# Performance work log

Hardware: AMD Instinct MI355X
Metric: run time of the kernel (lower is better)

## Reference

```python
import jax, jax.numpy as jnp
import numpy as np

N, E, R, B, H, C = 50000, 1600000, 50, 30, 16, 4


def setup_inputs() -> dict:
    key = jax.random.key(0)
    ks = jax.random.split(key, 12)
    edge_index = jax.random.randint(ks[0], (2, E), 0, N, dtype=jnp.int64)
    edge_type = jax.random.randint(ks[1], (E,), 0, R, dtype=jnp.int64)
    edge_norm = jax.random.uniform(ks[2], (E,), dtype=jnp.float32)
    s = 0.1
    basis1 = jax.random.normal(ks[3], (B, N, H), dtype=jnp.float32) * s
    comp1 = jax.random.normal(ks[4], (R, B), dtype=jnp.float32) * s
    root1 = jax.random.normal(ks[5], (N, H), dtype=jnp.float32) * s
    bias1 = jnp.zeros((H,), dtype=jnp.float32)
    basis2 = jax.random.normal(ks[6], (B, H, C), dtype=jnp.float32) * s
    comp2 = jax.random.normal(ks[7], (R, B), dtype=jnp.float32) * s
    root2 = jax.random.normal(ks[8], (H, C), dtype=jnp.float32) * s
    bias2 = jnp.zeros((C,), dtype=jnp.float32)
    return {
        "edge_index": edge_index, "edge_type": edge_type, "edge_norm": edge_norm,
        "basis1": basis1, "comp1": comp1, "root1": root1, "bias1": bias1,
        "basis2": basis2, "comp2": comp2, "root2": root2, "bias2": bias2,
    }


def _scatter_mean(msg, dst, n):
    # mean aggregation over destination nodes (PyG RGCNConv aggr='mean')
    summed = jnp.zeros((n, msg.shape[1]), dtype=msg.dtype).at[dst].add(msg)
    cnt = jnp.zeros((n,), dtype=msg.dtype).at[dst].add(1.0)
    return summed / jnp.maximum(cnt, 1.0)[:, None]


def reference(edge_index, edge_type, edge_norm, basis1, comp1, root1, bias1,
              basis2, comp2, root2, bias2):
    # edge_norm is accepted but unused, matching the original forward
    src, dst = edge_index[0], edge_index[1]
    n = root1.shape[0]
    # ---- layer 1: x is None -> per-(relation, src-node) weight row lookup ----
    w1 = jnp.einsum('rb,bnh->rnh', comp1, basis1)       # [R, N, H]
    msg1 = w1[edge_type, src]                           # [E, H] gather
    x = _scatter_mean(msg1, dst, n) + root1 + bias1      # root added directly (x=None)
    x = jax.nn.relu(x)
    # ---- layer 2: standard basis-decomposed RGCN on dense features ----
    w2 = jnp.einsum('rb,bhc->rhc', comp2, basis2)       # [R, H, C]
    msg2 = jnp.einsum('eh,ehc->ec', x[src], w2[edge_type])  # per-edge transform
    out = _scatter_mean(msg2, dst, n) + x @ root2 + bias2
    return jax.nn.log_softmax(out, axis=1)
```

## Files before the change

### kernel.cpp

```cpp
#include <hip/hip_runtime.h>
#include <math.h>

#define N_NODES 50000
#define E_EDGES 1600000
#define R_REL   50
#define B_BAS   30
#define H_DIM   16
#define C_DIM   4
#define NH      (N_NODES * H_DIM)

#define NSLICE      8
#define SLICE_NODES (N_NODES / NSLICE)

#define FRONT_BLOCKS (NH / 256)
#define EDGES_PER_FRONT (E_EDGES / FRONT_BLOCKS)

__global__ __launch_bounds__(256) void k_front(const float* __restrict__ basis1,
                                               const float* __restrict__ comp1,
                                               float* __restrict__ w1,
                                               const int* __restrict__ ei,
                                               int* __restrict__ cnt_i) {
    {
        const int ebase = blockIdx.x * EDGES_PER_FRONT + threadIdx.x;
        atomicAdd(&cnt_i[ei[E_EDGES + ebase]], 1);
        atomicAdd(&cnt_i[ei[E_EDGES + ebase + 256]], 1);
    }

    const int idx = blockIdx.x * 256 + threadIdx.x;
    float bv[B_BAS];
#pragma unroll
    for (int b = 0; b < B_BAS; ++b) bv[b] = basis1[b * NH + idx];

    for (int r = 0; r < R_REL; ++r) {
        float acc = 0.f;
#pragma unroll
        for (int b = 0; b < B_BAS; ++b) acc += comp1[r * B_BAS + b] * bv[b];
        w1[(size_t)r * NH + idx] = acc;
    }
}

__global__ __launch_bounds__(256) void k_scan_part(const int* __restrict__ cnt_i,
                                                   int* __restrict__ part,
                                                   int* __restrict__ bsum) {
    const int i = blockIdx.x * 256 + threadIdx.x;
    const int lane = threadIdx.x & 63;
    const int wid = threadIdx.x >> 6;
    const int v = (i < N_NODES) ? cnt_i[i] : 0;
    int s = v;
#pragma unroll
    for (int d = 1; d < 64; d <<= 1) {
        int t = __shfl_up(s, d, 64);
        if (lane >= d) s += t;
    }
    __shared__ int wsum[4];
    if (lane == 63) wsum[wid] = s;
    __syncthreads();
    int woff = 0;
    for (int w = 0; w < wid; ++w) woff += wsum[w];
    if (i < N_NODES) part[i] = s - v + woff;
    if (threadIdx.x == 255) bsum[blockIdx.x] = woff + s;
}

__global__ __launch_bounds__(256) void k_scan_tops(const int* __restrict__ bsum,
                                                   int* __restrict__ boff,
                                                   const float* __restrict__ basis2,
                                                   const float* __restrict__ comp2,
                                                   float* __restrict__ w2) {
    const int NB = (N_NODES + 255) / 256;
    const int lane = threadIdx.x & 63;
    const int wid = threadIdx.x >> 6;
    const int v = (threadIdx.x < NB) ? bsum[threadIdx.x] : 0;
    int s = v;
#pragma unroll
    for (int d = 1; d < 64; d <<= 1) {
        int t = __shfl_up(s, d, 64);
        if (lane >= d) s += t;
    }
    __shared__ int wsum[4];
    if (lane == 63) wsum[wid] = s;
    __syncthreads();
    int woff = 0;
    for (int w = 0; w < wid; ++w) woff += wsum[w];
    if (threadIdx.x < NB) boff[threadIdx.x] = s - v + woff;

    const int HC = H_DIM * C_DIM;
    for (int idx = threadIdx.x; idx < R_REL * HC; idx += 256) {
        const int r = idx / HC;
        const int hc = idx % HC;
        float acc = 0.f;
#pragma unroll
        for (int b = 0; b < B_BAS; ++b)
            acc += comp2[r * B_BAS + b] * basis2[b * HC + hc];
        w2[idx] = acc;
    }
}

__global__ __launch_bounds__(256) void k_scan_add(const int* __restrict__ part,
                                                  const int* __restrict__ boff,
                                                  int* __restrict__ off,
                                                  int* __restrict__ cursor) {
    const int i = blockIdx.x * 256 + threadIdx.x;
    if (i < N_NODES) {
        const int o = part[i] + boff[blockIdx.x];
        off[i] = o;
        cursor[i] = o;
    }
    if (i == 0) off[N_NODES] = E_EDGES;
}

__global__ __launch_bounds__(256) void k_bucket(const int* __restrict__ ei,
                                                const int* __restrict__ et,
                                                int* __restrict__ cursor,
                                                unsigned* __restrict__ rec) {
    const int chunk = blockIdx.x >> 3;
    const int slice = blockIdx.x & (NSLICE - 1);
    const int lo = slice * SLICE_NODES;

    const int e = chunk * 256 + threadIdx.x;
    if (e >= E_EDGES) return;
    const int dst = __builtin_nontemporal_load(&ei[E_EDGES + e]);
    if ((unsigned)(dst - lo) >= (unsigned)SLICE_NODES) return;

    const int src = __builtin_nontemporal_load(&ei[e]);
    const int r = __builtin_nontemporal_load(&et[e]);
    const int pos = atomicAdd(&cursor[dst], 1);
    rec[pos] = (unsigned)src | ((unsigned)r << 16);
}

__global__ __launch_bounds__(256) void k_agg1x(const unsigned* __restrict__ rec,
                                               const int* __restrict__ off,
                                               const float* __restrict__ w1,
                                               const float* __restrict__ root1,
                                               const float* __restrict__ bias1,
                                               float* __restrict__ x) {
    const int wid = threadIdx.x >> 6;
    const int lane = threadIdx.x & 63;
    const int dst = blockIdx.x * 4 + wid;
    const int h = lane & 15;
    const int sub = lane >> 4;
    const int e0 = off[dst], e1 = off[dst + 1];

    float acc = 0.f;
    for (int e = e0 + sub; e < e1; e += 16) {
        unsigned p[4];
#pragma unroll
        for (int j = 0; j < 4; ++j) {
            const int ej = e + j * 4;
            p[j] = (ej < e1) ? rec[ej] : 0xFFFFFFFFu;
        }
#pragma unroll
        for (int j = 0; j < 4; ++j) {
            if (p[j] != 0xFFFFFFFFu) {
                const int src = (int)(p[j] & 0xFFFFu);
                const int r = (int)(p[j] >> 16);
                acc += w1[(size_t)r * NH + src * H_DIM + h];
            }
        }
    }
    acc += __shfl_xor(acc, 16, 64);
    acc += __shfl_xor(acc, 32, 64);

    if (sub == 0) {
        const float c = fmaxf((float)(e1 - e0), 1.f);
        const float v = acc / c + root1[dst * H_DIM + h] + bias1[h];
        x[dst * H_DIM + h] = fmaxf(v, 0.f);
    }
}

__global__ __launch_bounds__(256) void k_agg2out(const unsigned* __restrict__ rec,
                                                 const int* __restrict__ off,
                                                 const float* __restrict__ x,
                                                 const float* __restrict__ w2,
                                                 const float* __restrict__ root2,
                                                 const float* __restrict__ bias2,
                                                 float* __restrict__ out) {
    const int wid = threadIdx.x >> 6;
    const int lane = threadIdx.x & 63;
    const int dst = blockIdx.x * 4 + wid;
    const int h = lane & 15;
    const int sub = lane >> 4;
    const int e0 = off[dst], e1 = off[dst + 1];

    float a0 = 0.f, a1 = 0.f, a2 = 0.f, a3 = 0.f;
    for (int e = e0 + sub; e < e1; e += 16) {
        unsigned p[4];
#pragma unroll
        for (int j = 0; j < 4; ++j) {
            const int ej = e + j * 4;
            p[j] = (ej < e1) ? rec[ej] : 0xFFFFFFFFu;
        }
#pragma unroll
        for (int j = 0; j < 4; ++j) {
            if (p[j] != 0xFFFFFFFFu) {
                const int src = (int)(p[j] & 0xFFFFu);
                const int r = (int)(p[j] >> 16);
                const float xv = x[src * H_DIM + h];
                const float4 w = *(const float4*)(w2 + r * (H_DIM * C_DIM) + h * C_DIM);
                a0 += xv * w.x; a1 += xv * w.y; a2 += xv * w.z; a3 += xv * w.w;
            }
        }
    }
#pragma unroll
    for (int d = 1; d < 64; d <<= 1) {
        a0 += __shfl_xor(a0, d, 64);
        a1 += __shfl_xor(a1, d, 64);
        a2 += __shfl_xor(a2, d, 64);
        a3 += __shfl_xor(a3, d, 64);
    }

    if (lane == 0) {
        const float c = fmaxf((float)(e1 - e0), 1.f);
        float y0 = a0 / c + bias2[0];
        float y1 = a1 / c + bias2[1];
        float y2 = a2 / c + bias2[2];
        float y3 = a3 / c + bias2[3];
#pragma unroll
        for (int hh = 0; hh < H_DIM; ++hh) {
            const float xv = x[dst * H_DIM + hh];
            const float4 w = *(const float4*)(root2 + hh * C_DIM);
            y0 += xv * w.x; y1 += xv * w.y; y2 += xv * w.z; y3 += xv * w.w;
        }
        const float m = fmaxf(fmaxf(y0, y1), fmaxf(y2, y3));
        const float s = expf(y0 - m) + expf(y1 - m) + expf(y2 - m) + expf(y3 - m);
        const float lse = m + logf(s);
        out[dst * 4 + 0] = y0 - lse;
        out[dst * 4 + 1] = y1 - lse;
        out[dst * 4 + 2] = y2 - lse;
        out[dst * 4 + 3] = y3 - lse;
    }
}

extern "C" void kernel_launch(void* const* d_in, const int* in_sizes, int n_in,
                              void* d_out, int out_size, void* d_ws, size_t ws_size,
                              hipStream_t stream) {
    const int*   edge_index = (const int*)d_in[0];
    const int*   edge_type  = (const int*)d_in[1];
    const float* basis1 = (const float*)d_in[3];
    const float* comp1  = (const float*)d_in[4];
    const float* root1  = (const float*)d_in[5];
    const float* bias1  = (const float*)d_in[6];
    const float* basis2 = (const float*)d_in[7];
    const float* comp2  = (const float*)d_in[8];
    const float* root2  = (const float*)d_in[9];
    const float* bias2  = (const float*)d_in[10];

    float* out = (float*)d_out;

    char* ws = (char*)d_ws;
    size_t o = 0;
    auto take = [&](size_t bytes) { char* p = ws + o; o += (bytes + 15) & ~(size_t)15; return p; };

    float*    w1     = (float*)   take((size_t)R_REL * NH * sizeof(float));
    unsigned* rec    = (unsigned*)take((size_t)E_EDGES * sizeof(unsigned));
    float*    x      = (float*)   take((size_t)NH * sizeof(float));
    int*      part   = (int*)x;
    int*      off    = (int*)     take((size_t)(N_NODES + 1) * sizeof(int));
    int*      cnt_i  = (int*)     take((size_t)N_NODES * sizeof(int));
    int*      cursor = (int*)     take((size_t)N_NODES * sizeof(int));
    float*    w2     = (float*)   take((size_t)R_REL * H_DIM * C_DIM * sizeof(float));
    int*      bsum   = (int*)     take(256 * sizeof(int));
    int*      boff   = (int*)     take(256 * sizeof(int));
    (void)ws_size;

    const int NB = (N_NODES + 255) / 256;

    hipMemsetAsync(cnt_i, 0, (size_t)N_NODES * sizeof(int), stream);

    k_front<<<FRONT_BLOCKS, 256, 0, stream>>>(basis1, comp1, w1, edge_index, cnt_i);

    k_scan_part<<<NB, 256, 0, stream>>>(cnt_i, part, bsum);
    k_scan_tops<<<1, 256, 0, stream>>>(bsum, boff, basis2, comp2, w2);
    k_scan_add<<<NB, 256, 0, stream>>>(part, boff, off, cursor);
    {
        const int chunks = (E_EDGES + 255) / 256;
        k_bucket<<<chunks * NSLICE, 256, 0, stream>>>(edge_index, edge_type, cursor, rec);
    }

    k_agg1x<<<N_NODES / 4, 256, 0, stream>>>(rec, off, w1, root1, bias1, x);

    k_agg2out<<<N_NODES / 4, 256, 0, stream>>>(rec, off, x, w2, root2, bias2, out);
}
```

Baseline: 412.1 us.

## Vectorize w1 basis contraction with float4 and split relations across block groups

The front kernel now processes four elements per thread with float4 loads and stores, and splits the 50 relations into 5 groups of 10 handled by separate blocks. Each thread keeps 10 float4 accumulators and streams over the basis instead of holding all 30 basis values. The degree-count atomics are redistributed to match the new block count. The goal is wider memory transactions and more parallelism for the bandwidth-bound w1 write, at the cost of reading basis1 five times.

```diff
diff --git a/kernel.cpp b/kernel.cpp
--- a/kernel.cpp
+++ b/kernel.cpp
@@ -8,35 +8,60 @@
 #define H_DIM   16
 #define C_DIM   4
 #define NH      (N_NODES * H_DIM)
+#define NH4     (NH / 4)
 
 #define NSLICE      8
 #define SLICE_NODES (N_NODES / NSLICE)
 
-#define FRONT_BLOCKS (NH / 256)
-#define EDGES_PER_FRONT (E_EDGES / FRONT_BLOCKS)
-
-__global__ __launch_bounds__(256) void k_front(const float* __restrict__ basis1,
-                                               const float* __restrict__ comp1,
-                                               float* __restrict__ w1,
-                                               const int* __restrict__ ei,
-                                               int* __restrict__ cnt_i) {
+#define R_GROUPS     5
+#define R_PER_GROUP  10
+#define IDX_BLOCKS   ((NH4 + 255) / 256)
+#define FRONT_BLOCKS (IDX_BLOCKS * R_GROUPS)
+#define EPB          410
+
+__global__ __launch_bounds__(256, 8) void k_front(const float* __restrict__ basis1,
+                                                  const float* __restrict__ comp1,
+                                                  float* __restrict__ w1,
+                                                  const int* __restrict__ ei,
+                                                  int* __restrict__ cnt_i) {
     {
-        const int ebase = blockIdx.x * EDGES_PER_FRONT + threadIdx.x;
-        atomicAdd(&cnt_i[ei[E_EDGES + ebase]], 1);
-        atomicAdd(&cnt_i[ei[E_EDGES + ebase + 256]], 1);
-    }
-
-    const int idx = blockIdx.x * 256 + threadIdx.x;
-    float bv[B_BAS];
-#pragma unroll
-    for (int b = 0; b < B_BAS; ++b) bv[b] = basis1[b * NH + idx];
-
-    for (int r = 0; r < R_REL; ++r) {
-        float acc = 0.f;
-#pragma unroll
-        for (int b = 0; b < B_BAS; ++b) acc += comp1[r * B_BAS + b] * bv[b];
-        w1[(size_t)r * NH + idx] = acc;
-    }
+        const int ebase = blockIdx.x * EPB;
+#pragma unroll
+        for (int i = 0; i < 2; ++i) {
+            const int el = threadIdx.x + i * 256;
+            if (el < EPB) {
+                const int e = ebase + el;
+                if (e < E_EDGES) atomicAdd(&cnt_i[ei[E_EDGES + e]], 1);
+            }
+        }
+    }
+
+    const int g = blockIdx.x % R_GROUPS;
+    const int idx4 = (blockIdx.x / R_GROUPS) * 256 + threadIdx.x;
+    if (idx4 >= NH4) return;
+
+    const float* bp = basis1 + (size_t)idx4 * 4;
+    float* wp = w1 + (size_t)idx4 * 4;
+    const int r0 = g * R_PER_GROUP;
+
+    float4 acc[R_PER_GROUP];
+#pragma unroll
+    for (int rr = 0; rr < R_PER_GROUP; ++rr) acc[rr] = {0.f, 0.f, 0.f, 0.f};
+
+    for (int b = 0; b < B_BAS; ++b) {
+        const float4 bv = *(const float4*)(bp + (size_t)b * NH);
+#pragma unroll
+        for (int rr = 0; rr < R_PER_GROUP; ++rr) {
+            const float c = comp1[(r0 + rr) * B_BAS + b];
+            acc[rr].x += c * bv.x;
+            acc[rr].y += c * bv.y;
+            acc[rr].z += c * bv.z;
+            acc[rr].w += c * bv.w;
+        }
+    }
+#pragma unroll
+    for (int rr = 0; rr < R_PER_GROUP; ++rr)
+        *(float4*)(wp + (size_t)(r0 + rr) * NH) = acc[rr];
 }
 
 __global__ __launch_bounds__(256) void k_scan_part(const int* __restrict__ cnt_i,
```

Result: slower. 453.1 us (+9.9%).
